# Performance work log

Measured on AMD Instinct MI355X. Metric: run time of the kernel, lower is better.

## Reference

```python
import jax, jax.numpy as jnp
import numpy as np
import math

B, S, D = 2, 2048, 1024
H = 16
HD = D // H
SPARSITY = 0.8


def setup_inputs() -> dict:
    key = jax.random.key(0)
    ks = jax.random.split(key, 5)
    scale = 1.0 / math.sqrt(D)
    return {
        "hidden_states": jax.random.normal(ks[0], (B, S, D), dtype=jnp.float32),
        "Wq": jax.random.normal(ks[1], (D, D), dtype=jnp.float32) * scale,
        "bq": jnp.zeros((D,), dtype=jnp.float32),
        "Wk": jax.random.normal(ks[2], (D, D), dtype=jnp.float32) * scale,
        "bk": jnp.zeros((D,), dtype=jnp.float32),
        "Wv": jax.random.normal(ks[3], (D, D), dtype=jnp.float32) * scale,
        "bv": jnp.zeros((D,), dtype=jnp.float32),
        "Wo": jax.random.normal(ks[4], (D, D), dtype=jnp.float32) * scale,
        "bo": jnp.zeros((D,), dtype=jnp.float32),
    }


def reference(hidden_states, Wq, bq, Wk, bk, Wv, bv, Wo, bo):
    b, s, d = hidden_states.shape
    # projections (torch Linear: x @ W.T + b), split heads -> [b, h, s, hd]
    def proj(W, bias):
        y = hidden_states @ W.T + bias
        return y.reshape(b, s, H, HD).transpose(0, 2, 1, 3)

    q = proj(Wq, bq)
    k = proj(Wk, bk)
    v = proj(Wv, bv)

    # scaled dot-product scores [b, h, s, s]
    attn = jnp.einsum("bhqd,bhkd->bhqk", q, k) / math.sqrt(HD)

    # top-k threshold per query row (k-th largest == sort-descending[k-1])
    kk = max(int(s * (1.0 - SPARSITY)), 1)
    thr = jax.lax.top_k(attn, kk)[0][..., kk - 1:kk]  # [b, h, s, 1]
    attn = attn + jnp.where(attn < thr, jnp.float32(-10000.0), jnp.float32(0.0))

    attn = jax.nn.softmax(attn, axis=-1)
    out = jnp.einsum("bhqk,bhkd->bhqd", attn, v)  # [b, h, s, hd]
    out = out.transpose(0, 2, 1, 3).reshape(b, s, d)
    return out @ Wo.T + bo
```

## Files before the change

### kernel.cpp

```cpp
#include <hip/hip_runtime.h>
#include <math.h>

#define S_LEN 2048
#define NH 16
#define HDIM 64
#define BATCH 2
#define BHC 32
#define KK 409
#define DMODEL 1024

typedef __attribute__((ext_vector_type(8))) short bf16x8;
typedef __attribute__((ext_vector_type(4))) float f32x4;

#define SC_STR 1032
#define P_STR  2056
#define T_STR  40

__device__ __forceinline__ unsigned f2ord(float f) {
    unsigned u = __float_as_uint(f);
    return (u & 0x80000000u) ? ~u : (u | 0x80000000u);
}
__device__ __forceinline__ float ord2f(unsigned v) {
    unsigned u = (v & 0x80000000u) ? (v & 0x7fffffffu) : ~v;
    return __uint_as_float(u);
}
__device__ __forceinline__ unsigned short f2bf(float f) {
    unsigned u = __float_as_uint(f);
    u += 0x7fffu + ((u >> 16) & 1u);
    return (unsigned short)(u >> 16);
}
__device__ __forceinline__ float bf2f(unsigned short h) {
    return __uint_as_float(((unsigned)h) << 16);
}

__global__ __launch_bounds__(256)
void split32(const float* __restrict__ in, unsigned short* __restrict__ hi,
             unsigned short* __restrict__ lo, int n4)
{
    const int i = blockIdx.x * 256 + threadIdx.x;
    if (i < n4) {
        const float4 v = ((const float4*)in)[i];
        ushort4 h, l;
        h.x = f2bf(v.x); l.x = f2bf(v.x - bf2f(h.x));
        h.y = f2bf(v.y); l.y = f2bf(v.y - bf2f(h.y));
        h.z = f2bf(v.z); l.z = f2bf(v.z - bf2f(h.z));
        h.w = f2bf(v.w); l.w = f2bf(v.w - bf2f(h.w));
        ((ushort4*)hi)[i] = h;
        ((ushort4*)lo)[i] = l;
    }
}

__global__ __launch_bounds__(256)
void gemm_mfma(const unsigned short* __restrict__ Ah, const unsigned short* __restrict__ Al,
               const unsigned short* __restrict__ Bh, const unsigned short* __restrict__ Bl,
               const float* __restrict__ bias, void* __restrict__ out0,
               void* __restrict__ out1, int mode)
{
    __shared__ __align__(16) unsigned short sAh[128 * T_STR];
    __shared__ __align__(16) unsigned short sAl[128 * T_STR];
    __shared__ __align__(16) unsigned short sBh[64 * T_STR];
    __shared__ __align__(16) unsigned short sBl[64 * T_STR];

    const int tid  = threadIdx.x;
    const int lane = tid & 63;
    const int w    = tid >> 6;
    const int q15  = lane & 15;
    const int quad = lane >> 4;
    const int n0b = blockIdx.x * 64;
    const int m0b = blockIdx.y * 128;
    const int wm = (w >> 1) * 64;
    const int wn = (w & 1) * 32;

    const int ar0 = tid >> 2, aks0 = (tid & 3) * 8;
    const int ar1 = (tid + 256) >> 2, aks1 = aks0;
    const int br = tid >> 2, bks = (tid & 3) * 8;

    const unsigned short* gAh0 = Ah + (size_t)(m0b + ar0) * 1024 + aks0;
    const unsigned short* gAh1 = Ah + (size_t)(m0b + ar1) * 1024 + aks1;
    const unsigned short* gAl0 = Al + (size_t)(m0b + ar0) * 1024 + aks0;
    const unsigned short* gAl1 = Al + (size_t)(m0b + ar1) * 1024 + aks1;
    const unsigned short* gBh = Bh + (size_t)(n0b + br) * 1024 + bks;
    const unsigned short* gBl = Bl + (size_t)(n0b + br) * 1024 + bks;

    f32x4 acc[4][2];
#pragma unroll
    for (int mt = 0; mt < 4; ++mt)
#pragma unroll
        for (int nt = 0; nt < 2; ++nt) acc[mt][nt] = (f32x4){0.f, 0.f, 0.f, 0.f};

#pragma unroll 1
    for (int k0 = 0; k0 < 1024; k0 += 32) {
        const bf16x8 vah0 = *(const bf16x8*)(gAh0 + k0);
        const bf16x8 vah1 = *(const bf16x8*)(gAh1 + k0);
        const bf16x8 val0 = *(const bf16x8*)(gAl0 + k0);
        const bf16x8 val1 = *(const bf16x8*)(gAl1 + k0);
        const bf16x8 vbh  = *(const bf16x8*)(gBh + k0);
        const bf16x8 vbl  = *(const bf16x8*)(gBl + k0);
        __syncthreads();
        *(bf16x8*)(sAh + ar0 * T_STR + aks0) = vah0;
        *(bf16x8*)(sAh + ar1 * T_STR + aks1) = vah1;
        *(bf16x8*)(sAl + ar0 * T_STR + aks0) = val0;
        *(bf16x8*)(sAl + ar1 * T_STR + aks1) = val1;
        *(bf16x8*)(sBh + br * T_STR + bks) = vbh;
        *(bf16x8*)(sBl + br * T_STR + bks) = vbl;
        __syncthreads();

        bf16x8 fbh[2], fbl[2];
#pragma unroll
        for (int nt = 0; nt < 2; ++nt) {
            fbh[nt] = *(const bf16x8*)(sBh + (wn + nt * 16 + q15) * T_STR + quad * 8);
            fbl[nt] = *(const bf16x8*)(sBl + (wn + nt * 16 + q15) * T_STR + quad * 8);
        }
#pragma unroll
        for (int mt = 0; mt < 4; ++mt) {
            const bf16x8 fah = *(const bf16x8*)(sAh + (wm + mt * 16 + q15) * T_STR + quad * 8);
            const bf16x8 fal = *(const bf16x8*)(sAl + (wm + mt * 16 + q15) * T_STR + quad * 8);
#pragma unroll
            for (int nt = 0; nt < 2; ++nt) {
                acc[mt][nt] = __builtin_amdgcn_mfma_f32_16x16x32_bf16(fah, fbh[nt], acc[mt][nt], 0, 0, 0);
                acc[mt][nt] = __builtin_amdgcn_mfma_f32_16x16x32_bf16(fah, fbl[nt], acc[mt][nt], 0, 0, 0);
                acc[mt][nt] = __builtin_amdgcn_mfma_f32_16x16x32_bf16(fal, fbh[nt], acc[mt][nt], 0, 0, 0);
            }
        }
    }

#pragma unroll
    for (int nt = 0; nt < 2; ++nt) {
        const int n = n0b + wn + nt * 16 + q15;
        const float bv = bias[n];
#pragma unroll
        for (int mt = 0; mt < 4; ++mt) {
            const int mb = m0b + wm + mt * 16 + quad * 4;
#pragma unroll
            for (int rg = 0; rg < 4; ++rg) {
                const int m = mb + rg;
                const float o = acc[mt][nt][rg] + bv;
                if (mode == 0) {
                    ((float*)out0)[(size_t)m * 1024 + n] = o;
                } else {
                    const int b = m >> 11, s = m & 2047;
                    const int h = n >> 6, hd = n & 63;
                    const size_t base = ((size_t)((b * NH + h) * S_LEN + s)) * HDIM + hd;
                    if (mode == 3) {
                        ((unsigned short*)out0)[base] = f2bf(o);
                    } else {
                        const unsigned short oh = f2bf(o);
                        ((unsigned short*)out0)[base] = oh;
                        ((unsigned short*)out1)[base] = f2bf(o - bf2f(oh));
                    }
                }
            }
        }
    }
}

__global__ __launch_bounds__(256)
void transpose_v16(const unsigned short* __restrict__ V, unsigned short* __restrict__ Vt)
{
    __shared__ unsigned short t[64][72];
    const int tid = threadIdx.x;
    const int s0 = blockIdx.x * 64;
    const int bh = blockIdx.y;
    const unsigned short* Vb = V + (size_t)bh * S_LEN * HDIM;
#pragma unroll
    for (int i = 0; i < 4; ++i) {
        const int f = tid + i * 256;
        const int s = f >> 4;
        const int hq = (f & 15) * 4;
        const ushort4 v = *(const ushort4*)(Vb + (size_t)(s0 + s) * HDIM + hq);
        t[s][hq + 0] = v.x; t[s][hq + 1] = v.y; t[s][hq + 2] = v.z; t[s][hq + 3] = v.w;
    }
    __syncthreads();
    unsigned short* Vtb = Vt + (size_t)bh * HDIM * S_LEN;
#pragma unroll
    for (int i = 0; i < 4; ++i) {
        const int f = tid + i * 256;
        const int hd = f >> 4;
        const int sq = (f & 15) * 4;
        ushort4 v;
        v.x = t[sq + 0][hd]; v.y = t[sq + 1][hd];
        v.z = t[sq + 2][hd]; v.w = t[sq + 3][hd];
        *(ushort4*)(Vtb + (size_t)hd * S_LEN + s0 + sq) = v;
    }
}

__device__ __forceinline__ unsigned radix_select(const unsigned* u)
{
    unsigned T = 0;
#pragma unroll 1
    for (int b = 31; b >= 0; --b) {
        const unsigned X = T | (1u << b);
        int cnt = 0;
#pragma unroll
        for (int i = 0; i < 32; ++i)
            cnt += __builtin_popcountll(__ballot(u[i] >= X));
        if (cnt >= KK) {
            T = X;
            if (cnt == KK) {
                unsigned mn = 0xffffffffu;
#pragma unroll
                for (int i = 0; i < 32; ++i) {
                    const unsigned v = (u[i] >= X) ? u[i] : 0xffffffffu;
                    mn = v < mn ? v : mn;
                }
#pragma unroll
                for (int off = 32; off >= 1; off >>= 1) {
                    const unsigned o = (unsigned)__shfl_xor((int)mn, off);
                    mn = o < mn ? o : mn;
                }
                return mn;
            }
        }
    }
    return T;
}

__global__ __launch_bounds__(512, 4)
void attn_kernel(const unsigned short* __restrict__ Qh, const unsigned short* __restrict__ Ql,
                 const unsigned short* __restrict__ Kh, const unsigned short* __restrict__ Kl,
                 const unsigned short* __restrict__ Vt,
                 unsigned short* __restrict__ AOh, unsigned short* __restrict__ AOl)
{
    extern __shared__ __align__(16) char smem[];
    float* sc = (float*)smem;
    unsigned short* P = (unsigned short*)smem;
    float* Opart = (float*)smem;

    const int tid  = threadIdx.x;
    const int lane = tid & 63;
    const int w    = tid >> 6;
    const int q15  = lane & 15;
    const int quad = lane >> 4;
    const int l5   = lane >> 5;
    const int l31  = lane & 31;

    const int blk = blockIdx.x;
    const int bh  = (blk & 7) * 4 + ((blk >> 3) & 3);
    const int q0  = (blk >> 5) * 16;

    const size_t qrow = ((size_t)bh * S_LEN + q0 + q15) * HDIM;
    const bf16x8 bqh0 = *(const bf16x8*)(Qh + qrow + quad * 8);
    const bf16x8 bqh1 = *(const bf16x8*)(Qh + qrow + 32 + quad * 8);
    const bf16x8 bql0 = *(const bf16x8*)(Ql + qrow + quad * 8);
    const bf16x8 bql1 = *(const bf16x8*)(Ql + qrow + 32 + quad * 8);

    const size_t kbase = (size_t)bh * S_LEN * HDIM;
    const int r0 = 2 * w, r1 = 2 * w + 1;
    unsigned u0[32], u1[32];

#pragma unroll 1
    for (int half = 0; half < 2; ++half) {
        f32x4 acc[8];
#pragma unroll 2
        for (int t = 0; t < 8; ++t) {
            const int key = w * 256 + half * 128 + t * 16 + q15;
            const unsigned short* kh = Kh + kbase + (size_t)key * HDIM + quad * 8;
            const unsigned short* kl = Kl + kbase + (size_t)key * HDIM + quad * 8;
            const bf16x8 akh0 = *(const bf16x8*)(kh);
            const bf16x8 akh1 = *(const bf16x8*)(kh + 32);
            const bf16x8 akl0 = *(const bf16x8*)(kl);
            const bf16x8 akl1 = *(const bf16x8*)(kl + 32);
            f32x4 c = {0.f, 0.f, 0.f, 0.f};
            c = __builtin_amdgcn_mfma_f32_16x16x32_bf16(akh0, bqh0, c, 0, 0, 0);
            c = __builtin_amdgcn_mfma_f32_16x16x32_bf16(akh1, bqh1, c, 0, 0, 0);
            c = __builtin_amdgcn_mfma_f32_16x16x32_bf16(akh0, bql0, c, 0, 0, 0);
            c = __builtin_amdgcn_mfma_f32_16x16x32_bf16(akh1, bql1, c, 0, 0, 0);
            c = __builtin_amdgcn_mfma_f32_16x16x32_bf16(akl0, bqh0, c, 0, 0, 0);
            c = __builtin_amdgcn_mfma_f32_16x16x32_bf16(akl1, bqh1, c, 0, 0, 0);
            acc[t] = c * 0.125f;
        }
        if (half) __syncthreads();
#pragma unroll
        for (int t = 0; t < 8; ++t)
            *(f32x4*)(sc + q15 * SC_STR + w * 128 + t * 16 + quad * 4) = acc[t];
        __syncthreads();
        unsigned* d0 = u0 + half * 16;
        unsigned* d1 = u1 + half * 16;
#pragma unroll
        for (int i = 0; i < 4; ++i) {
            const f32x4 v0 = *(const f32x4*)(sc + r0 * SC_STR + i * 256 + lane * 4);
            d0[4 * i + 0] = f2ord(v0[0]); d0[4 * i + 1] = f2ord(v0[1]);
            d0[4 * i + 2] = f2ord(v0[2]); d0[4 * i + 3] = f2ord(v0[3]);
            const f32x4 v1 = *(const f32x4*)(sc + r1 * SC_STR + i * 256 + lane * 4);
            d1[4 * i + 0] = f2ord(v1[0]); d1[4 * i + 1] = f2ord(v1[1]);
            d1[4 * i + 2] = f2ord(v1[2]); d1[4 * i + 3] = f2ord(v1[3]);
        }
    }
    __syncthreads();

    float invd[2];
#pragma unroll 1
    for (int rr = 0; rr < 2; ++rr) {
        const unsigned* u = rr ? u1 : u0;
        const int r = rr ? r1 : r0;
        const unsigned T = radix_select(u);
        unsigned umx = 0;
#pragma unroll
        for (int i = 0; i < 32; ++i) umx = u[i] > umx ? u[i] : umx;
#pragma unroll
        for (int off = 32; off >= 1; off >>= 1) {
            const unsigned o = (unsigned)__shfl_xor((int)umx, off);
            umx = o > umx ? o : umx;
        }
        const float mx = ord2f(umx);
        float lsum = 0.f;
        unsigned short* Pr = P + r * P_STR;
#pragma unroll
        for (int h = 0; h < 2; ++h) {
#pragma unroll
            for (int i = 0; i < 4; ++i) {
                const unsigned a0 = u[h * 16 + 4 * i + 0];
                const unsigned a1 = u[h * 16 + 4 * i + 1];
                const unsigned a2 = u[h * 16 + 4 * i + 2];
                const unsigned a3 = u[h * 16 + 4 * i + 3];
                const float e0 = (a0 >= T) ? __expf(ord2f(a0) - mx) : 0.f;
                const float e1 = (a1 >= T) ? __expf(ord2f(a1) - mx) : 0.f;
                const float e2 = (a2 >= T) ? __expf(ord2f(a2) - mx) : 0.f;
                const float e3 = (a3 >= T) ? __expf(ord2f(a3) - mx) : 0.f;
                ushort4 pk;
                pk.x = f2bf(e0); pk.y = f2bf(e1); pk.z = f2bf(e2); pk.w = f2bf(e3);
                const int key = (2 * i + l5) * 256 + h * 128 + l31 * 4;
                *(ushort4*)(Pr + key) = pk;
                lsum += e0 + e1 + e2 + e3;
            }
        }
#pragma unroll
        for (int off = 32; off >= 1; off >>= 1) lsum += __shfl_xor(lsum, off);
        invd[rr] = 1.f / lsum;
    }
    __syncthreads();

    {
        f32x4 oacc[4];
#pragma unroll
        for (int ht = 0; ht < 4; ++ht) oacc[ht] = (f32x4){0.f, 0.f, 0.f, 0.f};
        const size_t vtb = (size_t)bh * HDIM * S_LEN;
#pragma unroll 2
        for (int ks = 0; ks < 8; ++ks) {
            const int key0 = w * 256 + ks * 32 + quad * 8;
            const bf16x8 ap = *(const bf16x8*)(P + q15 * P_STR + key0);
#pragma unroll
            for (int ht = 0; ht < 4; ++ht) {
                const int hd = ht * 16 + q15;
                const bf16x8 bv = *(const bf16x8*)(Vt + vtb + (size_t)hd * S_LEN + key0);
                oacc[ht] = __builtin_amdgcn_mfma_f32_16x16x32_bf16(ap, bv, oacc[ht], 0, 0, 0);
            }
        }
        __syncthreads();
#pragma unroll
        for (int ht = 0; ht < 4; ++ht)
#pragma unroll
            for (int rg = 0; rg < 4; ++rg)
                Opart[w * 1024 + (quad * 4 + rg) * 64 + ht * 16 + q15] = oacc[ht][rg];
    }
    __syncthreads();

    {
        float s0 = 0.f, s1 = 0.f;
#pragma unroll
        for (int ww = 0; ww < 8; ++ww) {
            s0 += Opart[ww * 1024 + r0 * 64 + lane];
            s1 += Opart[ww * 1024 + r1 * 64 + lane];
        }
        const int b = bh >> 4, h = bh & 15;
        const float o0 = s0 * invd[0];
        const float o1 = s1 * invd[1];
        const size_t i0 = ((size_t)(b * S_LEN + q0 + r0)) * DMODEL + h * HDIM + lane;
        const size_t i1 = ((size_t)(b * S_LEN + q0 + r1)) * DMODEL + h * HDIM + lane;
        const unsigned short h0 = f2bf(o0), h1 = f2bf(o1);
        AOh[i0] = h0; AOl[i0] = f2bf(o0 - bf2f(h0));
        AOh[i1] = h1; AOl[i1] = f2bf(o1 - bf2f(h1));
    }
}

extern "C" void kernel_launch(void* const* d_in, const int* in_sizes, int n_in,
                              void* d_out, int out_size, void* d_ws, size_t ws_size,
                              hipStream_t stream)
{
    const float* X  = (const float*)d_in[0];
    const float* Wq = (const float*)d_in[1];
    const float* bq = (const float*)d_in[2];
    const float* Wk = (const float*)d_in[3];
    const float* bk = (const float*)d_in[4];
    const float* Wv = (const float*)d_in[5];
    const float* bv = (const float*)d_in[6];
    const float* Wo = (const float*)d_in[7];
    const float* bo = (const float*)d_in[8];

    char* p = (char*)d_ws;
    const size_t NEL = (size_t)BHC * S_LEN * HDIM;
    unsigned short* Q16h = (unsigned short*)p; p += NEL * 2;
    unsigned short* Q16l = (unsigned short*)p; p += NEL * 2;
    unsigned short* K16h = (unsigned short*)p; p += NEL * 2;
    unsigned short* K16l = (unsigned short*)p; p += NEL * 2;
    unsigned short* Vb16 = (unsigned short*)p; p += NEL * 2;
    unsigned short* Vt16 = (unsigned short*)p; p += NEL * 2;
    unsigned short* Xh   = (unsigned short*)p; p += NEL * 2;
    unsigned short* Xl   = (unsigned short*)p; p += NEL * 2;
    unsigned short* AOh  = (unsigned short*)p; p += NEL * 2;
    unsigned short* AOl  = (unsigned short*)p; p += NEL * 2;
    unsigned short* Wqh  = (unsigned short*)p; p += DMODEL * DMODEL * 2;
    unsigned short* Wql  = (unsigned short*)p; p += DMODEL * DMODEL * 2;
    unsigned short* Wkh  = (unsigned short*)p; p += DMODEL * DMODEL * 2;
    unsigned short* Wkl  = (unsigned short*)p; p += DMODEL * DMODEL * 2;
    unsigned short* Wvh  = (unsigned short*)p; p += DMODEL * DMODEL * 2;
    unsigned short* Wvl  = (unsigned short*)p; p += DMODEL * DMODEL * 2;
    unsigned short* Woh  = (unsigned short*)p; p += DMODEL * DMODEL * 2;
    unsigned short* Wol  = (unsigned short*)p; p += DMODEL * DMODEL * 2;

    const int attn_lds = 16 * SC_STR * 4;
    hipFuncSetAttribute((const void*)attn_kernel,
                        hipFuncAttributeMaxDynamicSharedMemorySize, attn_lds);

    const int X4 = (int)(NEL / 4);
    const int W4 = DMODEL * DMODEL / 4;

    split32<<<(X4 + 255) / 256, 256, 0, stream>>>(X,  Xh,  Xl,  X4);
    split32<<<(W4 + 255) / 256, 256, 0, stream>>>(Wq, Wqh, Wql, W4);
    split32<<<(W4 + 255) / 256, 256, 0, stream>>>(Wk, Wkh, Wkl, W4);
    split32<<<(W4 + 255) / 256, 256, 0, stream>>>(Wv, Wvh, Wvl, W4);
    split32<<<(W4 + 255) / 256, 256, 0, stream>>>(Wo, Woh, Wol, W4);

    const dim3 ggrid(16, 32, 1);
    gemm_mfma<<<ggrid, 256, 0, stream>>>(Xh, Xl, Wqh, Wql, bq, Q16h, Q16l, 2);
    gemm_mfma<<<ggrid, 256, 0, stream>>>(Xh, Xl, Wkh, Wkl, bk, K16h, K16l, 2);
    gemm_mfma<<<ggrid, 256, 0, stream>>>(Xh, Xl, Wvh, Wvl, bv, Vb16, nullptr, 3);
    transpose_v16<<<dim3(32, 32, 1), 256, 0, stream>>>(Vb16, Vt16);

    attn_kernel<<<4096, 512, attn_lds, stream>>>(Q16h, Q16l, K16h, K16l, Vt16, AOh, AOl);

    gemm_mfma<<<ggrid, 256, 0, stream>>>(AOh, AOl, Woh, Wol, bo, d_out, nullptr, 0);
}
```

Baseline: 859.1 us.

## Interleave radix-select for both rows, prefetch V tiles, and deepen unrolling

The per-row radix select that ran once for each of the two rows a wave owns is replaced by one fused loop that computes both thresholds together. This interleaves the two ballot/popcount chains and halves the loop overhead. The first two k-steps of V tiles are prefetched into registers before the select, so global load latency hides behind the select work. The QK and PV loops are also unrolled further. Together these raise register pressure under launch_bounds(512,4), which could cause spills or reduce occupancy.

Result: slower. 938.1 us (+9.2%).

```diff
diff --git a/kernel.cpp b/kernel.cpp
--- a/kernel.cpp
+++ b/kernel.cpp
@@ -184,35 +184,20 @@
     }
 }
 
-__device__ __forceinline__ unsigned radix_select(const unsigned* u)
-{
-    unsigned T = 0;
-#pragma unroll 1
-    for (int b = 31; b >= 0; --b) {
-        const unsigned X = T | (1u << b);
-        int cnt = 0;
-#pragma unroll
-        for (int i = 0; i < 32; ++i)
-            cnt += __builtin_popcountll(__ballot(u[i] >= X));
-        if (cnt >= KK) {
-            T = X;
-            if (cnt == KK) {
-                unsigned mn = 0xffffffffu;
-#pragma unroll
-                for (int i = 0; i < 32; ++i) {
-                    const unsigned v = (u[i] >= X) ? u[i] : 0xffffffffu;
-                    mn = v < mn ? v : mn;
-                }
-#pragma unroll
-                for (int off = 32; off >= 1; off >>= 1) {
-                    const unsigned o = (unsigned)__shfl_xor((int)mn, off);
-                    mn = o < mn ? o : mn;
-                }
-                return mn;
-            }
-        }
-    }
-    return T;
+__device__ __forceinline__ unsigned minred(const unsigned* u, unsigned X)
+{
+    unsigned mn = 0xffffffffu;
+#pragma unroll
+    for (int i = 0; i < 32; ++i) {
+        const unsigned v = (u[i] >= X) ? u[i] : 0xffffffffu;
+        mn = v < mn ? v : mn;
+    }
+#pragma unroll
+    for (int off = 32; off >= 1; off >>= 1) {
+        const unsigned o = (unsigned)__shfl_xor((int)mn, off);
+        mn = o < mn ? o : mn;
+    }
+    return mn;
 }
 
 __global__ __launch_bounds__(512, 4)
@@ -251,7 +236,7 @@
 #pragma unroll 1
     for (int half = 0; half < 2; ++half) {
         f32x4 acc[8];
-#pragma unroll 2
+#pragma unroll 4
         for (int t = 0; t < 8; ++t) {
             const int key = w * 256 + half * 128 + t * 16 + q15;
             const unsigned short* kh = Kh + kbase + (size_t)key * HDIM + quad * 8;
@@ -288,21 +273,60 @@
     }
     __syncthreads();
 
+    const size_t vtb = (size_t)bh * HDIM * S_LEN;
+    bf16x8 vpre[8];
+#pragma unroll
+    for (int ks = 0; ks < 2; ++ks)
+#pragma unroll
+        for (int ht = 0; ht < 4; ++ht) {
+            const int key0 = w * 256 + ks * 32 + quad * 8;
+            vpre[ks * 4 + ht] = *(const bf16x8*)(Vt + vtb + (size_t)(ht * 16 + q15) * S_LEN + key0);
+        }
+
+    unsigned res0, res1;
+    {
+        unsigned T0 = 0, T1 = 0;
+        int done = 0;
+#pragma unroll 1
+        for (int b = 31; b >= 0; --b) {
+            const unsigned X0 = T0 | (1u << b);
+            const unsigned X1 = T1 | (1u << b);
+            int c0 = 0, c1 = 0;
+#pragma unroll
+            for (int i = 0; i < 32; ++i) {
+                c0 += __builtin_popcountll(__ballot(u0[i] >= X0));
+                c1 += __builtin_popcountll(__ballot(u1[i] >= X1));
+            }
+            if (!(done & 1) && c0 >= KK) { T0 = X0; if (c0 == KK) done |= 1; }
+            if (!(done & 2) && c1 >= KK) { T1 = X1; if (c1 == KK) done |= 2; }
+            if (done == 3) break;
+        }
+        res0 = (done & 1) ? minred(u0, T0) : T0;
+        res1 = (done & 2) ? minred(u1, T1) : T1;
+    }
+
+    unsigned um0 = 0, um1 = 0;
+#pragma unroll
+    for (int i = 0; i < 32; ++i) {
+        um0 = u0[i] > um0 ? u0[i] : um0;
+        um1 = u1[i] > um1 ? u1[i] : um1;
+    }
+#pragma unroll
+    for (int off = 32; off >= 1; off >>= 1) {
+        const unsigned o0 = (unsigned)__shfl_xor((int)um0, off);
+        um0 = o0 > um0 ? o0 : um0;
+        const unsigned o1 = (unsigned)__shfl_xor((int)um1, off);
+        um1 = o1 > um1 ? o1 : um1;
+    }
+    const float mx0 = ord2f(um0), mx1 = ord2f(um1);
+
     float invd[2];
 #pragma unroll 1
     for (int rr = 0; rr < 2; ++rr) {
         const unsigned* u = rr ? u1 : u0;
         const int r = rr ? r1 : r0;
-        const unsigned T = radix_select(u);
-        unsigned umx = 0;
-#pragma unroll
-        for (int i = 0; i < 32; ++i) umx = u[i] > umx ? u[i] : umx;
-#pragma unroll
-        for (int off = 32; off >= 1; off >>= 1) {
-            const unsigned o = (unsigned)__shfl_xor((int)umx, off);
-            umx = o > umx ? o : umx;
-        }
-        const float mx = ord2f(umx);
+        const unsigned T = rr ? res1 : res0;
+        const float mx = rr ? mx1 : mx0;
         float lsum = 0.f;
         unsigned short* Pr = P + r * P_STR;
 #pragma unroll
@@ -334,15 +358,15 @@
         f32x4 oacc[4];
 #pragma unroll
         for (int ht = 0; ht < 4; ++ht) oacc[ht] = (f32x4){0.f, 0.f, 0.f, 0.f};
-        const size_t vtb = (size_t)bh * HDIM * S_LEN;
-#pragma unroll 2
+#pragma unroll
         for (int ks = 0; ks < 8; ++ks) {
             const int key0 = w * 256 + ks * 32 + quad * 8;
             const bf16x8 ap = *(const bf16x8*)(P + q15 * P_STR + key0);
 #pragma unroll
             for (int ht = 0; ht < 4; ++ht) {
                 const int hd = ht * 16 + q15;
-                const bf16x8 bv = *(const bf16x8*)(Vt + vtb + (size_t)hd * S_LEN + key0);
+                const bf16x8 bv = (ks < 2) ? vpre[ks * 4 + ht]
+                                           : *(const bf16x8*)(Vt + vtb + (size_t)hd * S_LEN + key0);
                 oacc[ht] = __builtin_amdgcn_mfma_f32_16x16x32_bf16(ap, bv, oacc[ht], 0, 0, 0);
             }
         }
```

## Halve attention LDS footprint by processing scores and P in quarter/half chunks

Applied to the files above, without the earlier changes.

The score staging buffer is reduced to quarter-width chunks, and the probability matrix P is written and consumed in two key halves, with the PV MFMA interleaved per half. This roughly halves shared memory per block (about 66KB to 33KB), and launch bounds are raised to 8 waves per SIMD to allow more resident blocks. The cost is extra barriers, a different P layout, and tighter register pressure under the stricter launch bound, which may cause spills given the 64 per-thread score registers.

New measurement: 889.8 us. 1.04x slower.

```diff
diff --git a/kernel.cpp b/kernel.cpp
--- a/kernel.cpp
+++ b/kernel.cpp
@@ -12,9 +12,9 @@
 typedef __attribute__((ext_vector_type(8))) short bf16x8;
 typedef __attribute__((ext_vector_type(4))) float f32x4;
 
-#define SC_STR 1032
-#define P_STR  2056
-#define T_STR  40
+#define SC_STRQ 520
+#define P_STRH  1032
+#define T_STR   40
 
 __device__ __forceinline__ unsigned f2ord(float f) {
     unsigned u = __float_as_uint(f);
@@ -215,7 +215,7 @@
     return T;
 }
 
-__global__ __launch_bounds__(512, 4)
+__global__ __launch_bounds__(512, 8)
 void attn_kernel(const unsigned short* __restrict__ Qh, const unsigned short* __restrict__ Ql,
                  const unsigned short* __restrict__ Kh, const unsigned short* __restrict__ Kl,
                  const unsigned short* __restrict__ Vt,
@@ -231,8 +231,6 @@
     const int w    = tid >> 6;
     const int q15  = lane & 15;
     const int quad = lane >> 4;
-    const int l5   = lane >> 5;
-    const int l31  = lane & 31;
 
     const int blk = blockIdx.x;
     const int bh  = (blk & 7) * 4 + ((blk >> 3) & 3);
@@ -249,11 +247,11 @@
     unsigned u0[32], u1[32];
 
 #pragma unroll 1
-    for (int half = 0; half < 2; ++half) {
-        f32x4 acc[8];
-#pragma unroll 2
-        for (int t = 0; t < 8; ++t) {
-            const int key = w * 256 + half * 128 + t * 16 + q15;
+    for (int qtr = 0; qtr < 4; ++qtr) {
+        f32x4 acc[4];
+#pragma unroll
+        for (int t = 0; t < 4; ++t) {
+            const int key = w * 256 + qtr * 64 + t * 16 + q15;
             const unsigned short* kh = Kh + kbase + (size_t)key * HDIM + quad * 8;
             const unsigned short* kl = Kl + kbase + (size_t)key * HDIM + quad * 8;
             const bf16x8 akh0 = *(const bf16x8*)(kh);
@@ -269,31 +267,31 @@
             c = __builtin_amdgcn_mfma_f32_16x16x32_bf16(akl1, bqh1, c, 0, 0, 0);
             acc[t] = c * 0.125f;
         }
-        if (half) __syncthreads();
-#pragma unroll
-        for (int t = 0; t < 8; ++t)
-            *(f32x4*)(sc + q15 * SC_STR + w * 128 + t * 16 + quad * 4) = acc[t];
+        if (qtr) __syncthreads();
+#pragma unroll
+        for (int t = 0; t < 4; ++t)
+            *(f32x4*)(sc + q15 * SC_STRQ + w * 64 + t * 16 + quad * 4) = acc[t];
         __syncthreads();
-        unsigned* d0 = u0 + half * 16;
-        unsigned* d1 = u1 + half * 16;
-#pragma unroll
-        for (int i = 0; i < 4; ++i) {
-            const f32x4 v0 = *(const f32x4*)(sc + r0 * SC_STR + i * 256 + lane * 4);
+        unsigned* d0 = u0 + qtr * 8;
+        unsigned* d1 = u1 + qtr * 8;
+#pragma unroll
+        for (int i = 0; i < 2; ++i) {
+            const f32x4 v0 = *(const f32x4*)(sc + r0 * SC_STRQ + i * 256 + lane * 4);
             d0[4 * i + 0] = f2ord(v0[0]); d0[4 * i + 1] = f2ord(v0[1]);
             d0[4 * i + 2] = f2ord(v0[2]); d0[4 * i + 3] = f2ord(v0[3]);
-            const f32x4 v1 = *(const f32x4*)(sc + r1 * SC_STR + i * 256 + lane * 4);
+            const f32x4 v1 = *(const f32x4*)(sc + r1 * SC_STRQ + i * 256 + lane * 4);
             d1[4 * i + 0] = f2ord(v1[0]); d1[4 * i + 1] = f2ord(v1[1]);
             d1[4 * i + 2] = f2ord(v1[2]); d1[4 * i + 3] = f2ord(v1[3]);
         }
     }
     __syncthreads();
 
-    float invd[2];
+    unsigned Ts[2];
+    float mxs[2];
 #pragma unroll 1
     for (int rr = 0; rr < 2; ++rr) {
         const unsigned* u = rr ? u1 : u0;
-        const int r = rr ? r1 : r0;
-        const unsigned T = radix_select(u);
+        Ts[rr] = radix_select(u);
         unsigned umx = 0;
 #pragma unroll
         for (int i = 0; i < 32; ++i) umx = u[i] > umx ? u[i] : umx;
@@ -302,69 +300,79 @@
             const unsigned o = (unsigned)__shfl_xor((int)umx, off);
             umx = o > umx ? o : umx;
         }
-        const float mx = ord2f(umx);
-        float lsum = 0.f;
-        unsigned short* Pr = P + r * P_STR;
-#pragma unroll
-        for (int h = 0; h < 2; ++h) {
-#pragma unroll
-            for (int i = 0; i < 4; ++i) {
-                const unsigned a0 = u[h * 16 + 4 * i + 0];
-                const unsigned a1 = u[h * 16 + 4 * i + 1];
-                const unsigned a2 = u[h * 16 + 4 * i + 2];
-                const unsigned a3 = u[h * 16 + 4 * i + 3];
+        mxs[rr] = ord2f(umx);
+    }
+
+    const size_t vtb = (size_t)bh * HDIM * S_LEN;
+    float lsum[2] = {0.f, 0.f};
+    f32x4 oacc[4];
+#pragma unroll
+    for (int ht = 0; ht < 4; ++ht) oacc[ht] = (f32x4){0.f, 0.f, 0.f, 0.f};
+
+#pragma unroll 1
+    for (int h = 0; h < 2; ++h) {
+#pragma unroll 1
+        for (int rr = 0; rr < 2; ++rr) {
+            const unsigned* u = rr ? u1 : u0;
+            const int r = rr ? r1 : r0;
+            const unsigned T = Ts[rr];
+            const float mx = mxs[rr];
+            float ls = 0.f;
+            unsigned short* Pr = P + r * P_STRH;
+#pragma unroll
+            for (int qtr = 0; qtr < 4; ++qtr) {
+                const unsigned a0 = u[qtr * 8 + h * 4 + 0];
+                const unsigned a1 = u[qtr * 8 + h * 4 + 1];
+                const unsigned a2 = u[qtr * 8 + h * 4 + 2];
+                const unsigned a3 = u[qtr * 8 + h * 4 + 3];
                 const float e0 = (a0 >= T) ? __expf(ord2f(a0) - mx) : 0.f;
                 const float e1 = (a1 >= T) ? __expf(ord2f(a1) - mx) : 0.f;
                 const float e2 = (a2 >= T) ? __expf(ord2f(a2) - mx) : 0.f;
                 const float e3 = (a3 >= T) ? __expf(ord2f(a3) - mx) : 0.f;
                 ushort4 pk;
                 pk.x = f2bf(e0); pk.y = f2bf(e1); pk.z = f2bf(e2); pk.w = f2bf(e3);
-                const int key = (2 * i + l5) * 256 + h * 128 + l31 * 4;
-                *(ushort4*)(Pr + key) = pk;
-                lsum += e0 + e1 + e2 + e3;
+                *(ushort4*)(Pr + quad * 256 + qtr * 64 + q15 * 4) = pk;
+                ls += e0 + e1 + e2 + e3;
             }
-        }
-#pragma unroll
-        for (int off = 32; off >= 1; off >>= 1) lsum += __shfl_xor(lsum, off);
-        invd[rr] = 1.f / lsum;
-    }
-    __syncthreads();
-
-    {
-        f32x4 oacc[4];
-#pragma unroll
-        for (int ht = 0; ht < 4; ++ht) oacc[ht] = (f32x4){0.f, 0.f, 0.f, 0.f};
-        const size_t vtb = (size_t)bh * HDIM * S_LEN;
-#pragma unroll 2
-        for (int ks = 0; ks < 8; ++ks) {
-            const int key0 = w * 256 + ks * 32 + quad * 8;
-            const bf16x8 ap = *(const bf16x8*)(P + q15 * P_STR + key0);
+            lsum[rr] += ls;
+        }
+        __syncthreads();
+#pragma unroll
+        for (int ks = 0; ks < 4; ++ks) {
+            const int lk0 = 128 * w + ks * 32 + quad * 8;
+            const bf16x8 ap = *(const bf16x8*)(P + q15 * P_STRH + lk0);
 #pragma unroll
             for (int ht = 0; ht < 4; ++ht) {
                 const int hd = ht * 16 + q15;
-                const bf16x8 bv = *(const bf16x8*)(Vt + vtb + (size_t)hd * S_LEN + key0);
+                const bf16x8 bv = *(const bf16x8*)(Vt + vtb + (size_t)hd * S_LEN + h * 1024 + lk0);
                 oacc[ht] = __builtin_amdgcn_mfma_f32_16x16x32_bf16(ap, bv, oacc[ht], 0, 0, 0);
             }
         }
         __syncthreads();
-#pragma unroll
-        for (int ht = 0; ht < 4; ++ht)
-#pragma unroll
-            for (int rg = 0; rg < 4; ++rg)
-                Opart[w * 1024 + (quad * 4 + rg) * 64 + ht * 16 + q15] = oacc[ht][rg];
-    }
+    }
+
+#pragma unroll
+    for (int ht = 0; ht < 4; ++ht)
+#pragma unroll
+        for (int rg = 0; rg < 4; ++rg)
+            Opart[w * 1024 + (quad * 4 + rg) * 64 + ht * 16 + q15] = oacc[ht][rg];
     __syncthreads();
 
     {
         float s0 = 0.f, s1 = 0.f;
+#pragma unroll
+        for (int off = 32; off >= 1; off >>= 1) {
+            lsum[0] += __shfl_xor(lsum[0], off);
+            lsum[1] += __shfl_xor(lsum[1], off);
+        }
 #pragma unroll
         for (int ww = 0; ww < 8; ++ww) {
             s0 += Opart[ww * 1024 + r0 * 64 + lane];
             s1 += Opart[ww * 1024 + r1 * 64 + lane];
         }
         const int b = bh >> 4, h = bh & 15;
-        const float o0 = s0 * invd[0];
-        const float o1 = s1 * invd[1];
+        const float o0 = s0 / lsum[0];
+        const float o1 = s1 / lsum[1];
         const size_t i0 = ((size_t)(b * S_LEN + q0 + r0)) * DMODEL + h * HDIM + lane;
         const size_t i1 = ((size_t)(b * S_LEN + q0 + r1)) * DMODEL + h * HDIM + lane;
         const unsigned short h0 = f2bf(o0), h1 = f2bf(o1);
@@ -408,7 +416,7 @@
     unsigned short* Woh  = (unsigned short*)p; p += DMODEL * DMODEL * 2;
     unsigned short* Wol  = (unsigned short*)p; p += DMODEL * DMODEL * 2;
 
-    const int attn_lds = 16 * SC_STR * 4;
+    const int attn_lds = 16 * SC_STRQ * 4;
     hipFuncSetAttribute((const void*)attn_kernel,
                         hipFuncAttributeMaxDynamicSharedMemorySize, attn_lds);
 
```
